# Kernel optimization log

Hardware: AMD Instinct MI355X
Metric: run time of the kernel (lower is better)

Reference implementation:

```python
import jax, jax.numpy as jnp
import numpy as np

N = 50000
E = 400000
D = 256            # in_dim == out_dim for every branch
H = 8              # mulhead
DH = D // H        # 32
L = 2              # num_layer per branch
NUM_CLASS = 7
SUM_OUT = 5 * D    # classifier in_dim = 1280
EPS = 1e-9         # BatchNorm eps


def _bn(x):
    # BatchNorm1d training-mode forward (biased var), affine at init (gamma=1, beta=0)
    mu = jnp.mean(x, axis=0)
    var = jnp.var(x, axis=0)
    return (x - mu) / jnp.sqrt(var + EPS)


def _gat_layer(f, Ws, bs, Wn, bn_, a_s, a_n, row, col, vals):
    # f: [N, D]; Ws/Wn: [H, D, DH]; bs/bn_: [H, DH]; a_s/a_n: [H, DH]
    f_self = jax.nn.relu(jnp.einsum('nd,hdk->nhk', f, Ws) + bs)      # [N,H,DH]
    f_neigh = jax.nn.relu(jnp.einsum('nd,hdk->nhk', f, Wn) + bn_)    # [N,H,DH]
    att_s = jax.nn.leaky_relu(jnp.einsum('nhk,hk->nh', f_self, a_s), 0.2)  # [N,H]
    # NOTE: original code computes attention_neigh from f_self (faithful)
    att_n = jax.nn.leaky_relu(jnp.einsum('nhk,hk->nh', f_self, a_n), 0.2)  # [N,H]
    e_att = (att_s[row] + att_n[col]) * vals[:, None]                # [E,H]
    msg = e_att[:, :, None] * f_neigh[col]                           # [E,H,DH]
    out = jax.ops.segment_sum(msg, row, num_segments=N)              # [N,H,DH]
    return out.reshape(N, H * DH)                                    # head concat


def _gat(f, Ws, bs, Wn, bn_, a_s, a_n, row, col, vals):
    for i in range(L):
        f = _bn(_gat_layer(f, Ws[i], bs[i], Wn[i], bn_[i], a_s[i], a_n[i], row, col, vals))
    return f


def _gcn(f, W, b, row, col, vals):
    for i in range(L):
        h = f @ W[i] + b[i]
        agg = jax.ops.segment_sum(vals[:, None] * h[col], row, num_segments=N)
        f = _bn(jax.nn.relu(agg))
    return f


def setup_inputs() -> dict:
    key = jax.random.key(0)
    ks = jax.random.split(key, 20)

    def xavier(k, shape):
        fan_in, fan_out = shape[-2], shape[-1]
        lim = float(np.sqrt(6.0 / (fan_in + fan_out)))
        return jax.random.uniform(k, shape, jnp.float32, -lim, lim)

    return {
        'f_in': jax.random.normal(ks[0], (N, D), jnp.float32),
        'edge_rows': jax.random.randint(ks[1], (4, E), 0, N, jnp.int64 if jax.config.jax_enable_x64 else jnp.int32),
        'edge_cols': jax.random.randint(ks[2], (4, E), 0, N, jnp.int64 if jax.config.jax_enable_x64 else jnp.int32),
        'edge_vals': jax.random.uniform(ks[3], (4, E), jnp.float32),
        # GAT params: [L, H, D, DH] / [L, H, DH]
        'gat_Ws': xavier(ks[4], (L, H, D, DH)),
        'gat_bs': jnp.zeros((L, H, DH), jnp.float32),
        'gat_Wn': xavier(ks[5], (L, H, D, DH)),
        'gat_bn': jnp.zeros((L, H, DH), jnp.float32),
        'gat_as': jnp.ones((L, H, DH), jnp.float32),   # init.ones_
        'gat_an': jnp.ones((L, H, DH), jnp.float32),
        # 3 vanilla GCN branches: [3, L, D, D] / [3, L, D]
        'gcn_W': xavier(ks[6], (3, L, D, D)),
        'gcn_b': jnp.zeros((3, L, D), jnp.float32),
        # self perceptron
        'self_W': xavier(ks[7], (D, D)),
        'self_b': jnp.zeros((D,), jnp.float32),
        # classifier
        'cls_W': xavier(ks[8], (SUM_OUT, NUM_CLASS)),
        'cls_b': jnp.zeros((NUM_CLASS,), jnp.float32),
    }


def reference(f_in, edge_rows, edge_cols, edge_vals,
              gat_Ws, gat_bs, gat_Wn, gat_bn, gat_as, gat_an,
              gcn_W, gcn_b, self_W, self_b, cls_W, cls_b):
    outs = []
    # fcgat branch (adj 0)
    outs.append(_gat(f_in, gat_Ws, gat_bs, gat_Wn, gat_bn, gat_as, gat_an,
                     edge_rows[0], edge_cols[0], edge_vals[0]))
    # uttr/past/futr vanilla GCN branches (adjs 1..3)
    for g in range(3):
        outs.append(_gcn(f_in, gcn_W[g], gcn_b[g],
                         edge_rows[g + 1], edge_cols[g + 1], edge_vals[g + 1]))
    # self perceptron (act=True -> relu + BN)
    outs.append(_bn(jax.nn.relu(f_in @ self_W + self_b)))
    f = jnp.concatenate(outs, axis=1)          # [N, 1280]
    return f @ cls_W + cls_b                   # classifier: act=False
```

## Files before the change

### kernel.cpp

```cpp
#include <hip/hip_runtime.h>


constexpr int D     = 256;
constexpr int NHEAD = 8;
constexpr int NCLS  = 7;
constexpr int NSLOT = 8;
constexpr float BN_EPS = 1e-9f;

typedef short  s16x8 __attribute__((ext_vector_type(8)));
typedef float  f32x4 __attribute__((ext_vector_type(4)));

__device__ __forceinline__ unsigned short f2bf(float f) {
  unsigned int u = __builtin_bit_cast(unsigned int, f);
  u += 0x7FFFu + ((u >> 16) & 1u);
  return (unsigned short)(u >> 16);
}
__device__ __forceinline__ float bf2f(unsigned short h) {
  unsigned int u = ((unsigned int)h) << 16;
  return __builtin_bit_cast(float, u);
}

__device__ __forceinline__ void gload_lds16(const void* g, void* l) {
  __builtin_amdgcn_global_load_lds(
      (const __attribute__((address_space(1))) unsigned int*)g,
      (__attribute__((address_space(3))) unsigned int*)l, 16, 0, 0);
}

__launch_bounds__(256)
__global__ void k_gemm_mfma(const unsigned short* __restrict__ A,
                            const unsigned short* __restrict__ Wt,
                            const float* __restrict__ bias,
                            const float* __restrict__ biasB,
                            unsigned short* __restrict__ C,
                            int M, int doRelu,
                            const float* __restrict__ a_s, const float* __restrict__ a_n,
                            float* __restrict__ attS, float* __restrict__ attN,
                            float* __restrict__ bnOut)
{
  __shared__ unsigned short As[128 * 32];
  __shared__ unsigned short Bs[128 * 32];
  const int t = threadIdx.x;
  const int wave = t >> 6, lane = t & 63;
  const int quad = lane >> 4, l16 = lane & 15;
  const int wm = (wave & 1) * 64, wn = (wave >> 1) * 64;
  const int bm = blockIdx.x * 128, bn = blockIdx.y * 128;

  f32x4 acc[4][4] = {};

  const int rA0 = wave * 32 + (lane >> 2);
  const int rA1 = rA0 + 16;
  const int sub = (lane & 3) * 8;
  const unsigned short* gA0 = A  + (size_t)min(bm + rA0, M - 1) * D + sub;
  const unsigned short* gA1 = A  + (size_t)min(bm + rA1, M - 1) * D + sub;
  const unsigned short* gB0 = Wt + (size_t)(bn + rA0) * D + sub;
  const unsigned short* gB1 = Wt + (size_t)(bn + rA1) * D + sub;
  unsigned short* lA0 = &As[wave * 1024];
  unsigned short* lA1 = &As[wave * 1024 + 512];
  unsigned short* lB0 = &Bs[wave * 1024];
  unsigned short* lB1 = &Bs[wave * 1024 + 512];

  for (int k0 = 0; k0 < D; k0 += 32) {
    gload_lds16(gA0 + k0, lA0);
    gload_lds16(gA1 + k0, lA1);
    gload_lds16(gB0 + k0, lB0);
    gload_lds16(gB1 + k0, lB1);
    __syncthreads();
    s16x8 af[4], bf[4];
#pragma unroll
    for (int mi = 0; mi < 4; ++mi)
      af[mi] = *(const s16x8*)(&As[(wm + mi * 16 + l16) * 32 + quad * 8]);
#pragma unroll
    for (int nj = 0; nj < 4; ++nj)
      bf[nj] = *(const s16x8*)(&Bs[(wn + nj * 16 + l16) * 32 + quad * 8]);
#pragma unroll
    for (int mi = 0; mi < 4; ++mi)
#pragma unroll
      for (int nj = 0; nj < 4; ++nj)
        acc[mi][nj] = __builtin_amdgcn_mfma_f32_16x16x32_bf16(af[mi], bf[nj], acc[mi][nj], 0, 0, 0);
    __syncthreads();
  }

  const bool attSlab = (attS != nullptr) && (bn < 256);
  if (attSlab) {
    const int hb = (bn + wn) >> 5;
#pragma unroll
    for (int mi = 0; mi < 4; ++mi) {
#pragma unroll
      for (int h = 0; h < 2; ++h) {
        float ps[4] = {}, pn[4] = {};
#pragma unroll
        for (int j = 0; j < 2; ++j) {
          const int nj = h * 2 + j;
          const int col = bn + wn + nj * 16 + l16;
          const float bv = bias[col];
          const float av = a_s[col], nv = a_n[col];
#pragma unroll
          for (int r = 0; r < 4; ++r) {
            const float v = fmaxf(acc[mi][nj][r] + bv, 0.f);
            ps[r] = fmaf(v, av, ps[r]);
            pn[r] = fmaf(v, nv, pn[r]);
          }
        }
#pragma unroll
        for (int m = 1; m < 16; m <<= 1)
#pragma unroll
          for (int r = 0; r < 4; ++r) {
            ps[r] += __shfl_xor(ps[r], m);
            pn[r] += __shfl_xor(pn[r], m);
          }
        if (l16 == 0) {
#pragma unroll
          for (int r = 0; r < 4; ++r) {
            const int row = bm + wm + mi * 16 + quad * 4 + r;
            if (row < M) {
              const float s_ = ps[r], n_ = pn[r];
              attS[(size_t)row * NHEAD + hb + h] = (s_ > 0.f) ? s_ : 0.2f * s_;
              attN[(size_t)row * NHEAD + hb + h] = (n_ > 0.f) ? n_ : 0.2f * n_;
            }
          }
        }
      }
    }
  } else {
    const int cBase = (attS != nullptr) ? 256 : 0;
    const float* bsrc = (attS != nullptr) ? biasB : bias;
    float cs[4] = {}, cq[4] = {};
#pragma unroll
    for (int nj = 0; nj < 4; ++nj) {
      const int col = bn + wn + nj * 16 + l16;
      const int cw  = col - cBase;
      const float bv = bsrc[cw];
#pragma unroll
      for (int mi = 0; mi < 4; ++mi) {
#pragma unroll
        for (int r = 0; r < 4; ++r) {
          const int row = bm + wm + mi * 16 + quad * 4 + r;
          if (row < M) {
            float v = acc[mi][nj][r] + bv;
            if (doRelu) v = fmaxf(v, 0.f);
            const unsigned short u = f2bf(v);
            C[(size_t)row * D + cw] = u;
            if (bnOut) {
              const float w = bf2f(u);
              cs[nj] += w;
              cq[nj] = fmaf(w, w, cq[nj]);
            }
          }
        }
      }
    }
    if (bnOut) {
#pragma unroll
      for (int nj = 0; nj < 4; ++nj) {
        cs[nj] += __shfl_xor(cs[nj], 16);
        cq[nj] += __shfl_xor(cq[nj], 16);
        cs[nj] += __shfl_xor(cs[nj], 32);
        cq[nj] += __shfl_xor(cq[nj], 32);
      }
      if (quad == 0) {
        float* slot = bnOut + (size_t)(blockIdx.x & (NSLOT - 1)) * 2 * D;
#pragma unroll
        for (int nj = 0; nj < 4; ++nj) {
          const int col = bn + wn + nj * 16 + l16;
          atomicAdd(&slot[col], cs[nj]);
          atomicAdd(&slot[D + col], cq[nj]);
        }
      }
    }
  }
}

__global__ void k_cvt(const float* __restrict__ src, unsigned short* __restrict__ dst, int n8)
{
  const int i = blockIdx.x * 256 + threadIdx.x;
  if (i >= n8) return;
  const float4 a = *(const float4*)(src + (size_t)i * 8);
  const float4 b = *(const float4*)(src + (size_t)i * 8 + 4);
  uint4 o;
  o.x = (unsigned)f2bf(a.x) | ((unsigned)f2bf(a.y) << 16);
  o.y = (unsigned)f2bf(a.z) | ((unsigned)f2bf(a.w) << 16);
  o.z = (unsigned)f2bf(b.x) | ((unsigned)f2bf(b.y) << 16);
  o.w = (unsigned)f2bf(b.z) | ((unsigned)f2bf(b.w) << 16);
  *(uint4*)(dst + (size_t)i * 8) = o;
}

__global__ void k_cvt_w(const float* __restrict__ gat_Ws, const float* __restrict__ gat_Wn,
                        const float* __restrict__ gcn_W, const float* __restrict__ self_W,
                        unsigned short* __restrict__ Wt)
{
  const int m = blockIdx.x >> 8, j = blockIdx.x & 255, d = threadIdx.x;
  float v;
  if (m < 4) {
    const int l = m >> 1;
    const float* W = (m & 1) ? gat_Wn : gat_Ws;
    v = W[(((size_t)l * NHEAD + (j >> 5)) * D + d) * 32 + (j & 31)];
  } else if (m < 10) {
    v = gcn_W[((size_t)(m - 4) * D + d) * D + j];
  } else {
    v = self_W[(size_t)d * D + j];
  }
  Wt[((size_t)m * D + j) * D + d] = f2bf(v);
}

__global__ void k_fold_w(const float* __restrict__ srcW, const float* __restrict__ srcB,
                         const float* __restrict__ sums, unsigned short* __restrict__ dstW,
                         float* __restrict__ dstB, int mode, int Nn)
{
  __shared__ float red[256];
  const int j = blockIdx.x;
  const int d = threadIdx.x;
  float sAcc = 0.f, qAcc = 0.f;
#pragma unroll
  for (int s8 = 0; s8 < NSLOT; ++s8) {
    sAcc += sums[s8 * 2 * D + d];
    qAcc += sums[s8 * 2 * D + D + d];
  }
  const float inv = 1.f / (float)Nn;
  const float m_ = sAcc * inv;
  const float rs = rsqrtf(qAcc * inv - m_ * m_ + BN_EPS);
  float w;
  if (mode == 0) w = srcW[(((size_t)(j >> 5)) * D + d) * 32 + (j & 31)];
  else           w = srcW[(size_t)d * D + j];
  const unsigned short q = f2bf(w * rs);
  dstW[(size_t)j * D + d] = q;
  red[d] = m_ * bf2f(q);
  __syncthreads();
  for (int off = 128; off > 0; off >>= 1) {
    if (d < off) red[d] += red[d + off];
    __syncthreads();
  }
  if (d == 0) dstB[j] = srcB[j] - red[0];
}

__global__ void k_count(const int* __restrict__ rows, int* __restrict__ cnt, int E4, int E, int N)
{
  const int i = blockIdx.x * 256 + threadIdx.x;
  if (i < E4) atomicAdd(&cnt[(i / E) * N + rows[i]], 1);
}

__global__ void k_scan_blk(const int* __restrict__ in, int* __restrict__ scanTmp,
                           int* __restrict__ blkSum, int n)
{
  __shared__ int buf[256];
  const int t = threadIdx.x, i = blockIdx.x * 256 + t;
  const int v = (i < n) ? in[i] : 0;
  buf[t] = v; __syncthreads();
  for (int off = 1; off < 256; off <<= 1) {
    const int x = (t >= off) ? buf[t - off] : 0;
    __syncthreads();
    buf[t] += x; __syncthreads();
  }
  if (i < n) scanTmp[i] = buf[t];
  if (t == 255) blkSum[blockIdx.x] = buf[255];
}

__global__ void k_scan_top(int* __restrict__ blkSum, int G)
{
  __shared__ int buf[1024];
  const int t = threadIdx.x;
  const int v = (t < G) ? blkSum[t] : 0;
  buf[t] = v; __syncthreads();
  for (int off = 1; off < 1024; off <<= 1) {
    const int x = (t >= off) ? buf[t - off] : 0;
    __syncthreads();
    buf[t] += x; __syncthreads();
  }
  if (t < G) blkSum[t] = buf[t] - v;
}

__global__ void k_scan_fin(const int* __restrict__ scanTmp, const int* __restrict__ blkOff,
                           int* __restrict__ rowptr, int n)
{
  const int i = blockIdx.x * 256 + threadIdx.x;
  if (i < n) rowptr[i + 1] = scanTmp[i] + blkOff[blockIdx.x];
  if (i == 0) rowptr[0] = 0;
}

__global__ void k_scatter(const int* __restrict__ rows, const int* __restrict__ cols,
                          const float* __restrict__ vals,
                          const int* __restrict__ rowptr, int* __restrict__ fill,
                          int2* __restrict__ edge, int E4, int E, int N)
{
  const int i = blockIdx.x * 256 + threadIdx.x;
  if (i >= E4) return;
  const int g = (i / E) * N + rows[i];
  const int p = rowptr[g] + atomicAdd(&fill[g], 1);
  edge[p] = make_int2(cols[i], __float_as_int(vals[i]));
}

__device__ __forceinline__ void acc8(float* a, uint4 f, float c) {
  const unsigned w[4] = {f.x, f.y, f.z, f.w};
#pragma unroll
  for (int k = 0; k < 4; ++k) {
    a[2 * k]     = fmaf(c, bf2f((unsigned short)(w[k] & 0xffff)), a[2 * k]);
    a[2 * k + 1] = fmaf(c, bf2f((unsigned short)(w[k] >> 16)),    a[2 * k + 1]);
  }
}

__device__ __forceinline__ uint4 pack8(const float* a, bool relu) {
  unsigned ov[4];
#pragma unroll
  for (int k = 0; k < 4; ++k) {
    float lo = a[2 * k], hi = a[2 * k + 1];
    if (relu) { lo = fmaxf(lo, 0.f); hi = fmaxf(hi, 0.f); }
    ov[k] = (unsigned)f2bf(lo) | ((unsigned)f2bf(hi) << 16);
  }
  uint4 o; o.x = ov[0]; o.y = ov[1]; o.z = ov[2]; o.w = ov[3];
  return o;
}

__global__ void k_gat_agg(const unsigned short* __restrict__ fneigh,
                          const float* __restrict__ attS, const float* __restrict__ attN,
                          const int* __restrict__ rowptr, const int2* __restrict__ edge,
                          unsigned short* __restrict__ out, int N)
{
  const int n = blockIdx.x * 4 + (threadIdx.x >> 6);
  if (n >= N) return;
  const int lane = threadIdx.x & 63;
  const int half = lane >> 5;
  const int c32  = lane & 31;
  const int head = c32 >> 2;
  const float as = attS[(size_t)n * NHEAD + head];
  float a[8] = {};
  int p = rowptr[n];
  const int e = rowptr[n + 1];
  for (; p + 3 < e; p += 4) {
    const int2 ea = edge[p + half];
    const int2 eb = edge[p + 2 + half];
    const float ca = (as + attN[(size_t)ea.x * NHEAD + head]) * __int_as_float(ea.y);
    const float cb = (as + attN[(size_t)eb.x * NHEAD + head]) * __int_as_float(eb.y);
    const uint4 fa = *(const uint4*)(fneigh + (size_t)ea.x * D + c32 * 8);
    const uint4 fb = *(const uint4*)(fneigh + (size_t)eb.x * D + c32 * 8);
    acc8(a, fa, ca);
    acc8(a, fb, cb);
  }
  if (p + 1 < e) {
    const int2 ea = edge[p + half];
    const float ca = (as + attN[(size_t)ea.x * NHEAD + head]) * __int_as_float(ea.y);
    const uint4 fa = *(const uint4*)(fneigh + (size_t)ea.x * D + c32 * 8);
    acc8(a, fa, ca);
    p += 2;
  }
  if (p < e && half == 0) {
    const int2 ea = edge[p];
    const float ca = (as + attN[(size_t)ea.x * NHEAD + head]) * __int_as_float(ea.y);
    const uint4 fa = *(const uint4*)(fneigh + (size_t)ea.x * D + c32 * 8);
    acc8(a, fa, ca);
  }
#pragma unroll
  for (int k = 0; k < 8; ++k) a[k] += __shfl_xor(a[k], 32);
  if (half == 0)
    *(uint4*)(out + (size_t)n * D + c32 * 8) = pack8(a, false);
}

__global__ void k_gcn_agg(const unsigned short* __restrict__ Hm,
                          const int* __restrict__ rowptr, const int2* __restrict__ edge,
                          unsigned short* __restrict__ out, int N)
{
  const int n = blockIdx.x * 4 + (threadIdx.x >> 6);
  if (n >= N) return;
  const int lane = threadIdx.x & 63;
  const int half = lane >> 5;
  const int c32  = lane & 31;
  float a[8] = {};
  int p = rowptr[n];
  const int e = rowptr[n + 1];
  for (; p + 3 < e; p += 4) {
    const int2 ea = edge[p + half];
    const int2 eb = edge[p + 2 + half];
    const uint4 fa = *(const uint4*)(Hm + (size_t)ea.x * D + c32 * 8);
    const uint4 fb = *(const uint4*)(Hm + (size_t)eb.x * D + c32 * 8);
    acc8(a, fa, __int_as_float(ea.y));
    acc8(a, fb, __int_as_float(eb.y));
  }
  if (p + 1 < e) {
    const int2 ea = edge[p + half];
    const uint4 fa = *(const uint4*)(Hm + (size_t)ea.x * D + c32 * 8);
    acc8(a, fa, __int_as_float(ea.y));
    p += 2;
  }
  if (p < e && half == 0) {
    const int2 ea = edge[p];
    const uint4 fa = *(const uint4*)(Hm + (size_t)ea.x * D + c32 * 8);
    acc8(a, fa, __int_as_float(ea.y));
  }
#pragma unroll
  for (int k = 0; k < 8; ++k) a[k] += __shfl_xor(a[k], 32);
  if (half == 0)
    *(uint4*)(out + (size_t)n * D + c32 * 8) = pack8(a, true);
}

__launch_bounds__(256)
__global__ void k_bn_stats(const unsigned short* __restrict__ X, float* __restrict__ sums, int M)
{
  __shared__ float ls[256][8];
  __shared__ float lq[256][8];
  const int t = threadIdx.x, cg = t & 31, rg = t >> 5;
  float s[8] = {}, q[8] = {};
  for (int r = blockIdx.x * 8 + rg; r < M; r += gridDim.x * 8) {
    const uint4 f = *(const uint4*)(X + (size_t)r * D + cg * 8);
    const unsigned w[4] = {f.x, f.y, f.z, f.w};
#pragma unroll
    for (int k = 0; k < 4; ++k) {
      const float lo = bf2f((unsigned short)(w[k] & 0xffff));
      const float hi = bf2f((unsigned short)(w[k] >> 16));
      s[2 * k]     += lo; q[2 * k]     = fmaf(lo, lo, q[2 * k]);
      s[2 * k + 1] += hi; q[2 * k + 1] = fmaf(hi, hi, q[2 * k + 1]);
    }
  }
#pragma unroll
  for (int k = 0; k < 8; ++k) { ls[t][k] = s[k]; lq[t][k] = q[k]; }
  __syncthreads();
  if (rg == 0) {
    float* slot = sums + (size_t)(blockIdx.x & (NSLOT - 1)) * 2 * D;
#pragma unroll
    for (int g = 1; g < 8; ++g)
#pragma unroll
      for (int k = 0; k < 8; ++k) { s[k] += ls[cg + 32 * g][k]; q[k] += lq[cg + 32 * g][k]; }
#pragma unroll
    for (int k = 0; k < 8; ++k) {
      atomicAdd(&slot[cg * 8 + k], s[k]);
      atomicAdd(&slot[D + cg * 8 + k], q[k]);
    }
  }
}

__global__ void k_classifier(const unsigned short* __restrict__ F, const float* __restrict__ W,
                             const float* __restrict__ sums, const float* __restrict__ cls_b,
                             float* __restrict__ out, int N, int baseRow, int initMode)
{
  __shared__ float smu[D], srs[D];
  const int t = threadIdx.x;
  {
    float sAcc = 0.f, qAcc = 0.f;
#pragma unroll
    for (int s8 = 0; s8 < NSLOT; ++s8) {
      sAcc += sums[s8 * 2 * D + t];
      qAcc += sums[s8 * 2 * D + D + t];
    }
    const float inv = 1.f / (float)N;
    const float m_ = sAcc * inv;
    smu[t] = m_;
    srs[t] = rsqrtf(qAcc * inv - m_ * m_ + BN_EPS);
  }
  __syncthreads();

  const int n = blockIdx.x * 8 + (t >> 5);
  if (n >= N) return;
  const int lane = t & 31;
  const uint4 f = *(const uint4*)(F + (size_t)n * D + lane * 8);
  const unsigned w[4] = {f.x, f.y, f.z, f.w};
  float fv[8];
#pragma unroll
  for (int k = 0; k < 4; ++k) {
    fv[2 * k]     = (bf2f((unsigned short)(w[k] & 0xffff)) - smu[lane * 8 + 2 * k])     * srs[lane * 8 + 2 * k];
    fv[2 * k + 1] = (bf2f((unsigned short)(w[k] >> 16))    - smu[lane * 8 + 2 * k + 1]) * srs[lane * 8 + 2 * k + 1];
  }
  const float* Wr = W + (size_t)(baseRow + lane * 8) * NCLS;
  float p[NCLS];
#pragma unroll
  for (int c = 0; c < NCLS; ++c) {
    float s = 0.f;
#pragma unroll
    for (int k = 0; k < 8; ++k) s = fmaf(fv[k], Wr[k * NCLS + c], s);
    p[c] = s;
  }
#pragma unroll
  for (int m = 1; m < 32; m <<= 1)
#pragma unroll
    for (int c = 0; c < NCLS; ++c) p[c] += __shfl_xor(p[c], m);
  if (lane == 0) {
    float* o = out + (size_t)n * NCLS;
    if (initMode) {
#pragma unroll
      for (int c = 0; c < NCLS; ++c) o[c] = p[c] + cls_b[c];
    } else {
#pragma unroll
      for (int c = 0; c < NCLS; ++c) o[c] += p[c];
    }
  }
}

extern "C" void kernel_launch(void* const* d_in, const int* in_sizes, int n_in,
                              void* d_out, int out_size, void* d_ws, size_t ws_size,
                              hipStream_t stream)
{
  const float* f_in   = (const float*)d_in[0];
  const int*   erow   = (const int*)d_in[1];
  const int*   ecol   = (const int*)d_in[2];
  const float* eval   = (const float*)d_in[3];
  const float* gat_Ws = (const float*)d_in[4];
  const float* gat_bs = (const float*)d_in[5];
  const float* gat_Wn = (const float*)d_in[6];
  const float* gat_bn = (const float*)d_in[7];
  const float* gat_as = (const float*)d_in[8];
  const float* gat_an = (const float*)d_in[9];
  const float* gcn_W  = (const float*)d_in[10];
  const float* gcn_b  = (const float*)d_in[11];
  const float* self_W = (const float*)d_in[12];
  const float* self_b = (const float*)d_in[13];
  const float* cls_W  = (const float*)d_in[14];
  const float* cls_b  = (const float*)d_in[15];
  float* out = (float*)d_out;

  const int N  = in_sizes[0] / D;
  const int E  = in_sizes[1] / 4;
  const int E4 = 4 * E, N4 = 4 * N;
  const size_t ND = (size_t)N * D;

  unsigned short* bufA = (unsigned short*)d_ws;
  unsigned short* bufB = bufA + ND;
  unsigned short* bufC = bufB + ND;
  unsigned short* finB = bufC + ND;
  unsigned short* Wt   = finB + ND;
  float* attS   = (float*)(Wt + (size_t)11 * D * D);
  float* attN   = attS + (size_t)N * NHEAD;
  int*   scanTmp= (int*)(attN + (size_t)N * NHEAD);
  int*   blkSum = scanTmp + N4;
  int*   rowptr = blkSum + 1024;
  int2*  edge   = (int2*)(rowptr + (N4 + 4));
  int*   cnt    = (int*)(edge + E4);
  int*   fill   = cnt + N4;
  float* foldB    = (float*)scanTmp;
  float* slotSums = (float*)scanTmp + 2048;
  const size_t zero_bytes = (size_t)(2 * N4) * sizeof(int);
  const size_t slot_bytes = (size_t)9 * NSLOT * 2 * D * sizeof(float);

  const dim3 gemm_grid((N + 127) / 128, D / 128);
  const dim3 gemm_grid2((N + 127) / 128, 4);
  const int nb8   = (N + 7) / 8;
  const int nb4   = (N + 3) / 4;
  const int scanG = (N4 + 255) / 256;

  hipMemsetAsync(cnt, 0, zero_bytes, stream);

  k_cvt  <<<(int)(ND / 8 + 255) / 256, 256, 0, stream>>>(f_in, finB, (int)(ND / 8));
  k_cvt_w<<<11 * 256, 256, 0, stream>>>(gat_Ws, gat_Wn, gcn_W, self_W, Wt);

  k_count   <<<(E4 + 255) / 256, 256, 0, stream>>>(erow, cnt, E4, E, N);
  k_scan_blk<<<scanG, 256, 0, stream>>>(cnt, scanTmp, blkSum, N4);
  k_scan_top<<<1, 1024, 0, stream>>>(blkSum, scanG);
  k_scan_fin<<<scanG, 256, 0, stream>>>(scanTmp, blkSum, rowptr, N4);
  k_scatter <<<(E4 + 255) / 256, 256, 0, stream>>>(erow, ecol, eval, rowptr, fill,
                                                   edge, E4, E, N);

  hipMemsetAsync(slotSums, 0, slot_bytes, stream);

  const size_t WM = (size_t)D * D;
  auto sumsOf = [&](int id) { return slotSums + (size_t)id * NSLOT * 2 * D; };
  auto stats = [&](unsigned short* X, int id) {
    k_bn_stats<<<256, 256, 0, stream>>>(X, sumsOf(id), N);
  };

  {
    const int* rp = rowptr;
    k_gemm_mfma<<<gemm_grid2, 256, 0, stream>>>(finB, Wt + 0 * WM, gat_bs, gat_bn,
                                                bufB, N, 1,
                                                gat_as, gat_an, attS, attN, nullptr);
    k_gat_agg  <<<nb4, 256, 0, stream>>>(bufB, attS, attN, rp, edge, bufC, N);
    stats(bufC, 0);
    k_fold_w<<<D, 256, 0, stream>>>(gat_Ws + (size_t)NHEAD * D * 32, gat_bs + D,
                                    sumsOf(0), Wt + 2 * WM, foldB + 0 * D, 0, N);
    k_fold_w<<<D, 256, 0, stream>>>(gat_Wn + (size_t)NHEAD * D * 32, gat_bn + D,
                                    sumsOf(0), Wt + 3 * WM, foldB + 1 * D, 0, N);
    k_gemm_mfma<<<gemm_grid2, 256, 0, stream>>>(bufC, Wt + 2 * WM, foldB + 0 * D,
                                                foldB + 1 * D, bufB, N, 1,
                                                gat_as + D, gat_an + D, attS, attN, nullptr);
    k_gat_agg  <<<nb4, 256, 0, stream>>>(bufB, attS, attN, rp, edge, bufA, N);
    stats(bufA, 1);
    k_classifier<<<nb8, 256, 0, stream>>>(bufA, cls_W, sumsOf(1), cls_b, out, N, 0, 1);
  }

  for (int g = 0; g < 3; ++g) {
    const int* rp = rowptr + (size_t)(g + 1) * N;
    const float* bg = gcn_b + (size_t)g * 2 * D;
    k_gemm_mfma<<<gemm_grid, 256, 0, stream>>>(finB, Wt + (4 + 2 * g) * WM, bg, bg,
                                               bufA, N, 0,
                                               nullptr, nullptr, nullptr, nullptr, nullptr);
    k_gcn_agg  <<<nb4, 256, 0, stream>>>(bufA, rp, edge, bufB, N);
    stats(bufB, 2 + 2 * g);
    k_fold_w<<<D, 256, 0, stream>>>(gcn_W + (size_t)(2 * g + 1) * D * D, bg + D,
                                    sumsOf(2 + 2 * g),
                                    Wt + (5 + 2 * g) * WM, foldB + (2 + g) * D, 1, N);
    k_gemm_mfma<<<gemm_grid, 256, 0, stream>>>(bufB, Wt + (5 + 2 * g) * WM,
                                               foldB + (2 + g) * D, foldB + (2 + g) * D,
                                               bufA, N, 0,
                                               nullptr, nullptr, nullptr, nullptr, nullptr);
    k_gcn_agg  <<<nb4, 256, 0, stream>>>(bufA, rp, edge, bufB, N);
    stats(bufB, 3 + 2 * g);
    k_classifier<<<nb8, 256, 0, stream>>>(bufB, cls_W, sumsOf(3 + 2 * g), cls_b,
                                          out, N, (1 + g) * D, 0);
  }

  k_gemm_mfma<<<gemm_grid, 256, 0, stream>>>(finB, Wt + 10 * WM, self_b, self_b,
                                             bufA, N, 1,
                                             nullptr, nullptr, nullptr, nullptr,
                                             sumsOf(8));
  k_classifier<<<nb8, 256, 0, stream>>>(bufA, cls_W, sumsOf(8), cls_b, out, N, 4 * D, 0);
}
```

Baseline: 1.171 ms.

## Fuse BatchNorm statistics into aggregation kernels and precollapse slot sums

The separate BN-stats pass, which re-read each aggregated bf16 matrix, is removed. Per-column sum and sum-of-squares are now computed inside the GAT/GCN aggregation epilogue and reduced per block into 64 atomic slots. A small collapse kernel turns the slots into mean and rsqrt once per branch, so each classifier block no longer re-reduces them. This saves one full read of the N×256 activation per layer, at the cost of many more atomics (one set per 4-row block) and a larger slot buffer aliased onto the count/fill scratch.

```diff
diff --git a/kernel.cpp b/kernel.cpp
--- a/kernel.cpp
+++ b/kernel.cpp
@@ -4,7 +4,7 @@
 constexpr int D     = 256;
 constexpr int NHEAD = 8;
 constexpr int NCLS  = 7;
-constexpr int NSLOT = 8;
+constexpr int NSLOT = 64;
 constexpr float BN_EPS = 1e-9f;
 
 typedef short  s16x8 __attribute__((ext_vector_type(8)));
@@ -210,10 +210,9 @@
   const int j = blockIdx.x;
   const int d = threadIdx.x;
   float sAcc = 0.f, qAcc = 0.f;
-#pragma unroll
   for (int s8 = 0; s8 < NSLOT; ++s8) {
-    sAcc += sums[s8 * 2 * D + d];
-    qAcc += sums[s8 * 2 * D + D + d];
+    sAcc += sums[(size_t)s8 * 2 * D + d];
+    qAcc += sums[(size_t)s8 * 2 * D + D + d];
   }
   const float inv = 1.f / (float)Nn;
   const float m_ = sAcc * inv;
@@ -232,6 +231,20 @@
   if (d == 0) dstB[j] = srcB[j] - red[0];
 }
 
+__global__ void k_collapse(const float* __restrict__ sums, float* __restrict__ murs, int Nn)
+{
+  const int t = threadIdx.x;
+  float sAcc = 0.f, qAcc = 0.f;
+  for (int s8 = 0; s8 < NSLOT; ++s8) {
+    sAcc += sums[(size_t)s8 * 2 * D + t];
+    qAcc += sums[(size_t)s8 * 2 * D + D + t];
+  }
+  const float inv = 1.f / (float)Nn;
+  const float m_ = sAcc * inv;
+  murs[t]     = m_;
+  murs[D + t] = rsqrtf(qAcc * inv - m_ * m_ + BN_EPS);
+}
+
 __global__ void k_count(const int* __restrict__ rows, int* __restrict__ cnt, int E4, int E, int N)
 {
   const int i = blockIdx.x * 256 + threadIdx.x;
@@ -297,152 +310,149 @@
   }
 }
 
-__device__ __forceinline__ uint4 pack8(const float* a, bool relu) {
-  unsigned ov[4];
-#pragma unroll
-  for (int k = 0; k < 4; ++k) {
-    float lo = a[2 * k], hi = a[2 * k + 1];
-    if (relu) { lo = fmaxf(lo, 0.f); hi = fmaxf(hi, 0.f); }
-    ov[k] = (unsigned)f2bf(lo) | ((unsigned)f2bf(hi) << 16);
-  }
-  uint4 o; o.x = ov[0]; o.y = ov[1]; o.z = ov[2]; o.w = ov[3];
-  return o;
+__device__ __forceinline__ void stats_reduce64(const float* s, const float* q,
+                                               float* __restrict__ sums)
+{
+  __shared__ float ls[128][8];
+  __shared__ float lq[128][8];
+  const int t = threadIdx.x;
+  const int c32 = t & 31;
+  if ((t & 32) == 0) {
+    const int idx = ((t >> 6) << 5) | c32;
+#pragma unroll
+    for (int k = 0; k < 8; ++k) { ls[idx][k] = s[k]; lq[idx][k] = q[k]; }
+  }
+  __syncthreads();
+  if (t < 32) {
+    float* slot = sums + (size_t)(blockIdx.x & (NSLOT - 1)) * 2 * D;
+#pragma unroll
+    for (int k = 0; k < 8; ++k) {
+      const float ss = ls[t][k] + ls[t + 32][k] + ls[t + 64][k] + ls[t + 96][k];
+      const float qq = lq[t][k] + lq[t + 32][k] + lq[t + 64][k] + lq[t + 96][k];
+      atomicAdd(&slot[t * 8 + k], ss);
+      atomicAdd(&slot[D + t * 8 + k], qq);
+    }
+  }
 }
 
 __global__ void k_gat_agg(const unsigned short* __restrict__ fneigh,
                           const float* __restrict__ attS, const float* __restrict__ attN,
                           const int* __restrict__ rowptr, const int2* __restrict__ edge,
-                          unsigned short* __restrict__ out, int N)
+                          unsigned short* __restrict__ out, float* __restrict__ sums, int N)
 {
   const int n = blockIdx.x * 4 + (threadIdx.x >> 6);
-  if (n >= N) return;
   const int lane = threadIdx.x & 63;
   const int half = lane >> 5;
   const int c32  = lane & 31;
   const int head = c32 >> 2;
-  const float as = attS[(size_t)n * NHEAD + head];
-  float a[8] = {};
-  int p = rowptr[n];
-  const int e = rowptr[n + 1];
-  for (; p + 3 < e; p += 4) {
-    const int2 ea = edge[p + half];
-    const int2 eb = edge[p + 2 + half];
-    const float ca = (as + attN[(size_t)ea.x * NHEAD + head]) * __int_as_float(ea.y);
-    const float cb = (as + attN[(size_t)eb.x * NHEAD + head]) * __int_as_float(eb.y);
-    const uint4 fa = *(const uint4*)(fneigh + (size_t)ea.x * D + c32 * 8);
-    const uint4 fb = *(const uint4*)(fneigh + (size_t)eb.x * D + c32 * 8);
-    acc8(a, fa, ca);
-    acc8(a, fb, cb);
-  }
-  if (p + 1 < e) {
-    const int2 ea = edge[p + half];
-    const float ca = (as + attN[(size_t)ea.x * NHEAD + head]) * __int_as_float(ea.y);
-    const uint4 fa = *(const uint4*)(fneigh + (size_t)ea.x * D + c32 * 8);
-    acc8(a, fa, ca);
-    p += 2;
-  }
-  if (p < e && half == 0) {
-    const int2 ea = edge[p];
-    const float ca = (as + attN[(size_t)ea.x * NHEAD + head]) * __int_as_float(ea.y);
-    const uint4 fa = *(const uint4*)(fneigh + (size_t)ea.x * D + c32 * 8);
-    acc8(a, fa, ca);
-  }
-#pragma unroll
-  for (int k = 0; k < 8; ++k) a[k] += __shfl_xor(a[k], 32);
-  if (half == 0)
-    *(uint4*)(out + (size_t)n * D + c32 * 8) = pack8(a, false);
+  float s[8] = {}, q[8] = {};
+  if (n < N) {
+    const float as = attS[(size_t)n * NHEAD + head];
+    float a[8] = {};
+    int p = rowptr[n];
+    const int e = rowptr[n + 1];
+    for (; p + 3 < e; p += 4) {
+      const int2 ea = edge[p + half];
+      const int2 eb = edge[p + 2 + half];
+      const float ca = (as + attN[(size_t)ea.x * NHEAD + head]) * __int_as_float(ea.y);
+      const float cb = (as + attN[(size_t)eb.x * NHEAD + head]) * __int_as_float(eb.y);
+      const uint4 fa = *(const uint4*)(fneigh + (size_t)ea.x * D + c32 * 8);
+      const uint4 fb = *(const uint4*)(fneigh + (size_t)eb.x * D + c32 * 8);
+      acc8(a, fa, ca);
+      acc8(a, fb, cb);
+    }
+    if (p + 1 < e) {
+      const int2 ea = edge[p + half];
+      const float ca = (as + attN[(size_t)ea.x * NHEAD + head]) * __int_as_float(ea.y);
+      const uint4 fa = *(const uint4*)(fneigh + (size_t)ea.x * D + c32 * 8);
+      acc8(a, fa, ca);
+      p += 2;
+    }
+    if (p < e && half == 0) {
+      const int2 ea = edge[p];
+      const float ca = (as + attN[(size_t)ea.x * NHEAD + head]) * __int_as_float(ea.y);
+      const uint4 fa = *(const uint4*)(fneigh + (size_t)ea.x * D + c32 * 8);
+      acc8(a, fa, ca);
+    }
+#pragma unroll
+    for (int k = 0; k < 8; ++k) a[k] += __shfl_xor(a[k], 32);
+    if (half == 0) {
+      unsigned ov[4];
+#pragma unroll
+      for (int k = 0; k < 4; ++k) {
+        const unsigned short ulo = f2bf(a[2 * k]), uhi = f2bf(a[2 * k + 1]);
+        ov[k] = (unsigned)ulo | ((unsigned)uhi << 16);
+        const float lo = bf2f(ulo), hi = bf2f(uhi);
+        s[2 * k]     = lo; q[2 * k]     = lo * lo;
+        s[2 * k + 1] = hi; q[2 * k + 1] = hi * hi;
+      }
+      uint4 o; o.x = ov[0]; o.y = ov[1]; o.z = ov[2]; o.w = ov[3];
+      *(uint4*)(out + (size_t)n * D + c32 * 8) = o;
+    }
+  }
+  stats_reduce64(s, q, sums);
 }
 
 __global__ void k_gcn_agg(const unsigned short* __restrict__ Hm,
                           const int* __restrict__ rowptr, const int2* __restrict__ edge,
-                          unsigned short* __restrict__ out, int N)
+                          unsigned short* __restrict__ out, float* __restrict__ sums, int N)
 {
   const int n = blockIdx.x * 4 + (threadIdx.x >> 6);
-  if (n >= N) return;
   const int lane = threadIdx.x & 63;
   const int half = lane >> 5;
   const int c32  = lane & 31;
-  float a[8] = {};
-  int p = rowptr[n];
-  const int e = rowptr[n + 1];
-  for (; p + 3 < e; p += 4) {
-    const int2 ea = edge[p + half];
-    const int2 eb = edge[p + 2 + half];
-    const uint4 fa = *(const uint4*)(Hm + (size_t)ea.x * D + c32 * 8);
-    const uint4 fb = *(const uint4*)(Hm + (size_t)eb.x * D + c32 * 8);
-    acc8(a, fa, __int_as_float(ea.y));
-    acc8(a, fb, __int_as_float(eb.y));
-  }
-  if (p + 1 < e) {
-    const int2 ea = edge[p + half];
-    const uint4 fa = *(const uint4*)(Hm + (size_t)ea.x * D + c32 * 8);
-    acc8(a, fa, __int_as_float(ea.y));
-    p += 2;
-  }
-  if (p < e && half == 0) {
-    const int2 ea = edge[p];
-    const uint4 fa = *(const uint4*)(Hm + (size_t)ea.x * D + c32 * 8);
-    acc8(a, fa, __int_as_float(ea.y));
-  }
-#pragma unroll
-  for (int k = 0; k < 8; ++k) a[k] += __shfl_xor(a[k], 32);
-  if (half == 0)
-    *(uint4*)(out + (size_t)n * D + c32 * 8) = pack8(a, true);
-}
-
-__launch_bounds__(256)
-__global__ void k_bn_stats(const unsigned short* __restrict__ X, float* __restrict__ sums, int M)
-{
-  __shared__ float ls[256][8];
-  __shared__ float lq[256][8];
-  const int t = threadIdx.x, cg = t & 31, rg = t >> 5;
   float s[8] = {}, q[8] = {};
-  for (int r = blockIdx.x * 8 + rg; r < M; r += gridDim.x * 8) {
-    const uint4 f = *(const uint4*)(X + (size_t)r * D + cg * 8);
-    const unsigned w[4] = {f.x, f.y, f.z, f.w};
-#pragma unroll
-    for (int k = 0; k < 4; ++k) {
-      const float lo = bf2f((unsigned short)(w[k] & 0xffff));
-      const float hi = bf2f((unsigned short)(w[k] >> 16));
-      s[2 * k]     += lo; q[2 * k]     = fmaf(lo, lo, q[2 * k]);
-      s[2 * k + 1] += hi; q[2 * k + 1] = fmaf(hi, hi, q[2 * k + 1]);
-    }
-  }
-#pragma unroll
-  for (int k = 0; k < 8; ++k) { ls[t][k] = s[k]; lq[t][k] = q[k]; }
-  __syncthreads();
-  if (rg == 0) {
-    float* slot = sums + (size_t)(blockIdx.x & (NSLOT - 1)) * 2 * D;
-#pragma unroll
-    for (int g = 1; g < 8; ++g)
-#pragma unroll
-      for (int k = 0; k < 8; ++k) { s[k] += ls[cg + 32 * g][k]; q[k] += lq[cg + 32 * g][k]; }
-#pragma unroll
-    for (int k = 0; k < 8; ++k) {
-      atomicAdd(&slot[cg * 8 + k], s[k]);
-      atomicAdd(&slot[D + cg * 8 + k], q[k]);
-    }
-  }
+  if (n < N) {
+    float a[8] = {};
+    int p = rowptr[n];
+    const int e = rowptr[n + 1];
+    for (; p + 3 < e; p += 4) {
+      const int2 ea = edge[p + half];
+      const int2 eb = edge[p + 2 + half];
+      const uint4 fa = *(const uint4*)(Hm + (size_t)ea.x * D + c32 * 8);
+      const uint4 fb = *(const uint4*)(Hm + (size_t)eb.x * D + c32 * 8);
+      acc8(a, fa, __int_as_float(ea.y));
+      acc8(a, fb, __int_as_float(eb.y));
+    }
+    if (p + 1 < e) {
+      const int2 ea = edge[p + half];
+      const uint4 fa = *(const uint4*)(Hm + (size_t)ea.x * D + c32 * 8);
+      acc8(a, fa, __int_as_float(ea.y));
+      p += 2;
+    }
+    if (p < e && half == 0) {
+      const int2 ea = edge[p];
+      const uint4 fa = *(const uint4*)(Hm + (size_t)ea.x * D + c32 * 8);
+      acc8(a, fa, __int_as_float(ea.y));
+    }
+#pragma unroll
+    for (int k = 0; k < 8; ++k) a[k] += __shfl_xor(a[k], 32);
+    if (half == 0) {
+      unsigned ov[4];
+#pragma unroll
+      for (int k = 0; k < 4; ++k) {
+        const float vlo = fmaxf(a[2 * k], 0.f), vhi = fmaxf(a[2 * k + 1], 0.f);
+        const unsigned short ulo = f2bf(vlo), uhi = f2bf(vhi);
+        ov[k] = (unsigned)ulo | ((unsigned)uhi << 16);
+        const float lo = bf2f(ulo), hi = bf2f(uhi);
+        s[2 * k]     = lo; q[2 * k]     = lo * lo;
+        s[2 * k + 1] = hi; q[2 * k + 1] = hi * hi;
+      }
+      uint4 o; o.x = ov[0]; o.y = ov[1]; o.z = ov[2]; o.w = ov[3];
+      *(uint4*)(out + (size_t)n * D + c32 * 8) = o;
+    }
+  }
+  stats_reduce64(s, q, sums);
 }
 
 __global__ void k_classifier(const unsigned short* __restrict__ F, const float* __restrict__ W,
-                             const float* __restrict__ sums, const float* __restrict__ cls_b,
+                             const float* __restrict__ murs, const float* __restrict__ cls_b,
                              float* __restrict__ out, int N, int baseRow, int initMode)
 {
   __shared__ float smu[D], srs[D];
   const int t = threadIdx.x;
-  {
-    float sAcc = 0.f, qAcc = 0.f;
-#pragma unroll
-    for (int s8 = 0; s8 < NSLOT; ++s8) {
-      sAcc += sums[s8 * 2 * D + t];
-      qAcc += sums[s8 * 2 * D + D + t];
-    }
-    const float inv = 1.f / (float)N;
-    const float m_ = sAcc * inv;
-    smu[t] = m_;
-    srs[t] = rsqrtf(qAcc * inv - m_ * m_ + BN_EPS);
-  }
+  smu[t] = murs[t];
+  srs[t] = murs[D + t];
   __syncthreads();
 
   const int n = blockIdx.x * 8 + (t >> 5);
@@ -522,7 +532,8 @@
   int*   cnt    = (int*)(edge + E4);
   int*   fill   = cnt + N4;
   float* foldB    = (float*)scanTmp;
-  float* slotSums = (float*)scanTmp + 2048;
+  float* murs     = (float*)scanTmp + 2048;
+  float* slotSums = (float*)cnt;
   const size_t zero_bytes = (size_t)(2 * N4) * sizeof(int);
   const size_t slot_bytes = (size_t)9 * NSLOT * 2 * D * sizeof(float);
 
@@ -548,17 +559,15 @@
 
   const size_t WM = (size_t)D * D;
   auto sumsOf = [&](int id) { return slotSums + (size_t)id * NSLOT * 2 * D; };
-  auto stats = [&](unsigned short* X, int id) {
-    k_bn_stats<<<256, 256, 0, stream>>>(X, sumsOf(id), N);
-  };
+  auto mursOf = [&](int id) { return murs + (size_t)id * 2 * D; };
 
   {
     const int* rp = rowptr;
     k_gemm_mfma<<<gemm_grid2, 256, 0, stream>>>(finB, Wt + 0 * WM, gat_bs, gat_bn,
                                                 bufB, N, 1,
                                                 gat_as, gat_an, attS, attN, nullptr);
-    k_gat_agg  <<<nb4, 256, 0, stream>>>(bufB, attS, attN, rp, edge, bufC, N);
-    stats(bufC, 0);
+    k_gat_agg  <<<nb4, 256, 0, stream>>>(bufB, attS, attN, rp, edge, bufC,
+                                         sumsOf(0), N);
     k_fold_w<<<D, 256, 0, stream>>>(gat_Ws + (size_t)NHEAD * D * 32, gat_bs + D,
                                     sumsOf(0), Wt + 2 * WM, foldB + 0 * D, 0, N);
     k_fold_w<<<D, 256, 0, stream>>>(gat_Wn + (size_t)NHEAD * D * 32, gat_bn + D,
@@ -566,9 +575,10 @@
     k_gemm_mfma<<<gemm_grid2, 256, 0, stream>>>(bufC, Wt + 2 * WM, foldB + 0 * D,
                                                 foldB + 1 * D, bufB, N, 1,
                                                 gat_as + D, gat_an + D, attS, attN, nullptr);
-    k_gat_agg  <<<nb4, 256, 0, stream>>>(bufB, attS, attN, rp, edge, bufA, N);
-    stats(bufA, 1);
-    k_classifier<<<nb8, 256, 0, stream>>>(bufA, cls_W, sumsOf(1), cls_b, out, N, 0, 1);
+    k_gat_agg  <<<nb4, 256, 0, stream>>>(bufB, attS, attN, rp, edge, bufA,
+                                         sumsOf(1), N);
+    k_collapse<<<1, 256, 0, stream>>>(sumsOf(1), mursOf(1), N);
+    k_classifier<<<nb8, 256, 0, stream>>>(bufA, cls_W, mursOf(1), cls_b, out, N, 0, 1);
   }
 
   for (int g = 0; g < 3; ++g) {
@@ -577,8 +587,7 @@
     k_gemm_mfma<<<gemm_grid, 256, 0, stream>>>(finB, Wt + (4 + 2 * g) * WM, bg, bg,
                                                bufA, N, 0,
                                                nullptr, nullptr, nullptr, nullptr, nullptr);
-    k_gcn_agg  <<<nb4, 256, 0, stream>>>(bufA, rp, edge, bufB, N);
-    stats(bufB, 2 + 2 * g);
+    k_gcn_agg  <<<nb4, 256, 0, stream>>>(bufA, rp, edge, bufB, sumsOf(2 + 2 * g), N);
     k_fold_w<<<D, 256, 0, stream>>>(gcn_W + (size_t)(2 * g + 1) * D * D, bg + D,
                                     sumsOf(2 + 2 * g),
                                     Wt + (5 + 2 * g) * WM, foldB + (2 + g) * D, 1, N);
@@ -586,9 +595,9 @@
                                                foldB + (2 + g) * D, foldB + (2 + g) * D,
                                                bufA, N, 0,
                                                nullptr, nullptr, nullptr, nullptr, nullptr);
-    k_gcn_agg  <<<nb4, 256, 0, stream>>>(bufA, rp, edge, bufB, N);
-    stats(bufB, 3 + 2 * g);
-    k_classifier<<<nb8, 256, 0, stream>>>(bufB, cls_W, sumsOf(3 + 2 * g), cls_b,
+    k_gcn_agg  <<<nb4, 256, 0, stream>>>(bufA, rp, edge, bufB, sumsOf(3 + 2 * g), N);
+    k_collapse<<<1, 256, 0, stream>>>(sumsOf(3 + 2 * g), mursOf(3 + 2 * g), N);
+    k_classifier<<<nb8, 256, 0, stream>>>(bufB, cls_W, mursOf(3 + 2 * g), cls_b,
                                           out, N, (1 + g) * D, 0);
   }
 
@@ -596,5 +605,6 @@
                                              bufA, N, 1,
                                              nullptr, nullptr, nullptr, nullptr,
                                              sumsOf(8));
-  k_classifier<<<nb8, 256, 0, stream>>>(bufA, cls_W, sumsOf(8), cls_b, out, N, 4 * D, 0);
-}
+  k_collapse<<<1, 256, 0, stream>>>(sumsOf(8), mursOf(8), N);
+  k_classifier<<<nb8, 256, 0, stream>>>(bufA, cls_W, mursOf(8), cls_b, out, N, 4 * D, 0);
+}
```

Measured after the change: 2.690 ms. 130% more time.

## Spread BN stats over more slots and blocks, tile weight transpose, precollapse stats

Applied to the files above, without the earlier changes.

Raises the number of partial-sum slots for batch-norm statistics from 8 to 64 and launches the stats kernel with 1024 blocks instead of 256, to cut atomic contention and add parallelism. Adds a single-block collapse kernel so each classifier block reads precomputed mean and rstd instead of every block re-summing all slots. Rewrites the weight conversion/transpose kernel to use a 32x32 shared-memory tile so both reads and writes are coalesced. The slot sums now live in the count buffer region, and the extra launches add small fixed overhead.

```diff
diff --git a/kernel.cpp b/kernel.cpp
--- a/kernel.cpp
+++ b/kernel.cpp
@@ -4,7 +4,7 @@
 constexpr int D     = 256;
 constexpr int NHEAD = 8;
 constexpr int NCLS  = 7;
-constexpr int NSLOT = 8;
+constexpr int NSLOT = 64;
 constexpr float BN_EPS = 1e-9f;
 
 typedef short  s16x8 __attribute__((ext_vector_type(8)));
@@ -188,18 +188,33 @@
                         const float* __restrict__ gcn_W, const float* __restrict__ self_W,
                         unsigned short* __restrict__ Wt)
 {
-  const int m = blockIdx.x >> 8, j = blockIdx.x & 255, d = threadIdx.x;
-  float v;
-  if (m < 4) {
-    const int l = m >> 1;
-    const float* W = (m & 1) ? gat_Wn : gat_Ws;
-    v = W[(((size_t)l * NHEAD + (j >> 5)) * D + d) * 32 + (j & 31)];
-  } else if (m < 10) {
-    v = gcn_W[((size_t)(m - 4) * D + d) * D + j];
-  } else {
-    v = self_W[(size_t)d * D + j];
-  }
-  Wt[((size_t)m * D + j) * D + d] = f2bf(v);
+  __shared__ float tile[32][33];
+  const int m = blockIdx.x, jt = blockIdx.y, dt = blockIdx.z;
+  const int tx = threadIdx.x & 31, ty = threadIdx.x >> 5;
+#pragma unroll
+  for (int r = 0; r < 4; ++r) {
+    const int dl = ty * 4 + r;
+    const int d  = dt * 32 + dl;
+    float v;
+    if (m < 4) {
+      const int l = m >> 1;
+      const float* W = (m & 1) ? gat_Wn : gat_Ws;
+      v = W[(((size_t)l * NHEAD + jt) * D + d) * 32 + tx];
+    } else if (m < 10) {
+      v = gcn_W[((size_t)(m - 4) * D + d) * D + jt * 32 + tx];
+    } else {
+      v = self_W[(size_t)d * D + jt * 32 + tx];
+    }
+    tile[dl][tx] = v;
+  }
+  __syncthreads();
+#pragma unroll
+  for (int r = 0; r < 4; ++r) {
+    const int jl = ty * 4 + r;
+    const int j  = jt * 32 + jl;
+    const int d  = dt * 32 + tx;
+    Wt[((size_t)m * D + j) * D + d] = f2bf(tile[tx][jl]);
+  }
 }
 
 __global__ void k_fold_w(const float* __restrict__ srcW, const float* __restrict__ srcB,
@@ -210,10 +225,9 @@
   const int j = blockIdx.x;
   const int d = threadIdx.x;
   float sAcc = 0.f, qAcc = 0.f;
-#pragma unroll
   for (int s8 = 0; s8 < NSLOT; ++s8) {
-    sAcc += sums[s8 * 2 * D + d];
-    qAcc += sums[s8 * 2 * D + D + d];
+    sAcc += sums[(size_t)s8 * 2 * D + d];
+    qAcc += sums[(size_t)s8 * 2 * D + D + d];
   }
   const float inv = 1.f / (float)Nn;
   const float m_ = sAcc * inv;
@@ -230,6 +244,20 @@
     __syncthreads();
   }
   if (d == 0) dstB[j] = srcB[j] - red[0];
+}
+
+__global__ void k_collapse(const float* __restrict__ sums, float* __restrict__ murs, int Nn)
+{
+  const int t = threadIdx.x;
+  float sAcc = 0.f, qAcc = 0.f;
+  for (int s8 = 0; s8 < NSLOT; ++s8) {
+    sAcc += sums[(size_t)s8 * 2 * D + t];
+    qAcc += sums[(size_t)s8 * 2 * D + D + t];
+  }
+  const float inv = 1.f / (float)Nn;
+  const float m_ = sAcc * inv;
+  murs[t]     = m_;
+  murs[D + t] = rsqrtf(qAcc * inv - m_ * m_ + BN_EPS);
 }
 
 __global__ void k_count(const int* __restrict__ rows, int* __restrict__ cnt, int E4, int E, int N)
@@ -426,23 +454,13 @@
 }
 
 __global__ void k_classifier(const unsigned short* __restrict__ F, const float* __restrict__ W,
-                             const float* __restrict__ sums, const float* __restrict__ cls_b,
+                             const float* __restrict__ murs, const float* __restrict__ cls_b,
                              float* __restrict__ out, int N, int baseRow, int initMode)
 {
   __shared__ float smu[D], srs[D];
   const int t = threadIdx.x;
-  {
-    float sAcc = 0.f, qAcc = 0.f;
-#pragma unroll
-    for (int s8 = 0; s8 < NSLOT; ++s8) {
-      sAcc += sums[s8 * 2 * D + t];
-      qAcc += sums[s8 * 2 * D + D + t];
-    }
-    const float inv = 1.f / (float)N;
-    const float m_ = sAcc * inv;
-    smu[t] = m_;
-    srs[t] = rsqrtf(qAcc * inv - m_ * m_ + BN_EPS);
-  }
+  smu[t] = murs[t];
+  srs[t] = murs[D + t];
   __syncthreads();
 
   const int n = blockIdx.x * 8 + (t >> 5);
@@ -522,12 +540,14 @@
   int*   cnt    = (int*)(edge + E4);
   int*   fill   = cnt + N4;
   float* foldB    = (float*)scanTmp;
-  float* slotSums = (float*)scanTmp + 2048;
+  float* murs     = (float*)scanTmp + 2048;
+  float* slotSums = (float*)cnt;
   const size_t zero_bytes = (size_t)(2 * N4) * sizeof(int);
   const size_t slot_bytes = (size_t)9 * NSLOT * 2 * D * sizeof(float);
 
   const dim3 gemm_grid((N + 127) / 128, D / 128);
   const dim3 gemm_grid2((N + 127) / 128, 4);
+  const dim3 cvtw_grid(11, 8, 8);
   const int nb8   = (N + 7) / 8;
   const int nb4   = (N + 3) / 4;
   const int scanG = (N4 + 255) / 256;
@@ -535,7 +555,7 @@
   hipMemsetAsync(cnt, 0, zero_bytes, stream);
 
   k_cvt  <<<(int)(ND / 8 + 255) / 256, 256, 0, stream>>>(f_in, finB, (int)(ND / 8));
-  k_cvt_w<<<11 * 256, 256, 0, stream>>>(gat_Ws, gat_Wn, gcn_W, self_W, Wt);
+  k_cvt_w<<<cvtw_grid, 256, 0, stream>>>(gat_Ws, gat_Wn, gcn_W, self_W, Wt);
 
   k_count   <<<(E4 + 255) / 256, 256, 0, stream>>>(erow, cnt, E4, E, N);
   k_scan_blk<<<scanG, 256, 0, stream>>>(cnt, scanTmp, blkSum, N4);
@@ -548,8 +568,9 @@
 
   const size_t WM = (size_t)D * D;
   auto sumsOf = [&](int id) { return slotSums + (size_t)id * NSLOT * 2 * D; };
+  auto mursOf = [&](int id) { return murs + (size_t)id * 2 * D; };
   auto stats = [&](unsigned short* X, int id) {
-    k_bn_stats<<<256, 256, 0, stream>>>(X, sumsOf(id), N);
+    k_bn_stats<<<1024, 256, 0, stream>>>(X, sumsOf(id), N);
   };
 
   {
@@ -568,7 +589,8 @@
                                                 gat_as + D, gat_an + D, attS, attN, nullptr);
     k_gat_agg  <<<nb4, 256, 0, stream>>>(bufB, attS, attN, rp, edge, bufA, N);
     stats(bufA, 1);
-    k_classifier<<<nb8, 256, 0, stream>>>(bufA, cls_W, sumsOf(1), cls_b, out, N, 0, 1);
+    k_collapse<<<1, 256, 0, stream>>>(sumsOf(1), mursOf(1), N);
+    k_classifier<<<nb8, 256, 0, stream>>>(bufA, cls_W, mursOf(1), cls_b, out, N, 0, 1);
   }
 
   for (int g = 0; g < 3; ++g) {
@@ -588,7 +610,8 @@
                                                nullptr, nullptr, nullptr, nullptr, nullptr);
     k_gcn_agg  <<<nb4, 256, 0, stream>>>(bufA, rp, edge, bufB, N);
     stats(bufB, 3 + 2 * g);
-    k_classifier<<<nb8, 256, 0, stream>>>(bufB, cls_W, sumsOf(3 + 2 * g), cls_b,
+    k_collapse<<<1, 256, 0, stream>>>(sumsOf(3 + 2 * g), mursOf(3 + 2 * g), N);
+    k_classifier<<<nb8, 256, 0, stream>>>(bufB, cls_W, mursOf(3 + 2 * g), cls_b,
                                           out, N, (1 + g) * D, 0);
   }
 
@@ -596,5 +619,6 @@
                                              bufA, N, 1,
                                              nullptr, nullptr, nullptr, nullptr,
                                              sumsOf(8));
-  k_classifier<<<nb8, 256, 0, stream>>>(bufA, cls_W, sumsOf(8), cls_b, out, N, 4 * D, 0);
-}
+  k_collapse<<<1, 256, 0, stream>>>(sumsOf(8), mursOf(8), N);
+  k_classifier<<<nb8, 256, 0, stream>>>(bufA, cls_W, mursOf(8), cls_b, out, N, 4 * D, 0);
+}
```

New measurement: 1.255 ms. 1.07x slower.
